# Performance work log

Measured on AMD Instinct MI355X. Metric: run time of the kernel, lower is better.

## Reference

```python
import jax, jax.numpy as jnp
import numpy as np

H = 512  # hidden size

def _lstm_layer(xseq, W_ih, W_hh, b_ih, b_hh):
    """xseq: [S,B,D]. Returns (h_seq [S,B,H], c_final [B,H]). PyTorch gate order i,f,g,o."""
    S, B, _ = xseq.shape
    # precompute input contribution for all timesteps: [S,B,4H]
    gx = jnp.einsum('sbd,gd->sbg', xseq, W_ih) + b_ih + b_hh
    h0 = jnp.zeros((B, H), xseq.dtype)
    c0 = jnp.zeros((B, H), xseq.dtype)

    def step(carry, gx_t):
        h, c = carry
        gates = gx_t + h @ W_hh.T  # [B,4H]
        i, f, g, o = jnp.split(gates, 4, axis=-1)
        c = jax.nn.sigmoid(f) * c + jax.nn.sigmoid(i) * jnp.tanh(g)
        h = jax.nn.sigmoid(o) * jnp.tanh(c)
        return (h, c), h

    (_, c_fin), h_seq = jax.lax.scan(step, (h0, c0), gx)
    return h_seq, c_fin


def setup_inputs() -> dict:
    key = jax.random.key(0)
    ks = jax.random.split(key, 12)
    V, D, L = 50257, 300, 10
    s = 0.08  # weight scale to keep gates in a sane range
    return {
        'x': jax.random.randint(ks[0], (64, 512), 0, V),
        'emb': jax.random.normal(ks[1], (V, D), jnp.float32),
        'W_ih0': s * jax.random.normal(ks[2], (4 * H, D), jnp.float32),
        'W_hh0': s * jax.random.normal(ks[3], (4 * H, H), jnp.float32),
        'b_ih0': s * jax.random.normal(ks[4], (4 * H,), jnp.float32),
        'b_hh0': s * jax.random.normal(ks[5], (4 * H,), jnp.float32),
        'W_ih1': s * jax.random.normal(ks[6], (4 * H, H), jnp.float32),
        'W_hh1': s * jax.random.normal(ks[7], (4 * H, H), jnp.float32),
        'b_ih1': s * jax.random.normal(ks[8], (4 * H,), jnp.float32),
        'b_hh1': s * jax.random.normal(ks[9], (4 * H,), jnp.float32),
        'W_out': s * jax.random.normal(ks[10], (L, H), jnp.float32),
        'b_out': s * jax.random.normal(ks[11], (L,), jnp.float32),
    }


def reference(x, emb, W_ih0, W_hh0, b_ih0, b_hh0, W_ih1, W_hh1, b_ih1, b_hh1, W_out, b_out):
    xe = emb[x]                      # [B,S,D] embedding gather
    xe = jnp.transpose(xe, (1, 0, 2))  # [S,B,D] time-major for scan
    h1, _ = _lstm_layer(xe, W_ih0, W_hh0, b_ih0, b_hh0)
    _, c2 = _lstm_layer(h1, W_ih1, W_hh1, b_ih1, b_hh1)  # c_n[-1]: [B,H]
    return c2 @ W_out.T + b_out      # [B,n_labels]
```

## Files before the change

kernel.cpp:

```cpp
#include <hip/hip_runtime.h>
#include <hip/hip_bf16.h>
#include <stdint.h>

#define BB 64
#define SS 512
#define HH 512
#define DD 300
#define DP 320

typedef __attribute__((ext_vector_type(8))) short short8;
typedef __attribute__((ext_vector_type(4))) float f32x4;

__device__ __forceinline__ unsigned short f2bf(float f) {
  unsigned u = __builtin_bit_cast(unsigned, f);
  u += 0x7fffu + ((u >> 16) & 1u);
  return (unsigned short)(u >> 16);
}
__device__ __forceinline__ float sigm(float x) { return 1.f / (1.f + __expf(-x)); }
__device__ __forceinline__ float tanh_f(float x) {
  float t = __expf(-2.f * fabsf(x));
  float r = (1.f - t) / (1.f + t);
  return x < 0.f ? -r : r;
}

__device__ __forceinline__ short8 load_frag_sc1(const unsigned short* p) {
  short8 r;
  asm volatile("global_load_dwordx4 %0, %1, off sc1" : "=v"(r) : "v"(p));
  return r;
}
__device__ __forceinline__ short8 load_frag(const unsigned short* p) {
  short8 r;
  asm volatile("global_load_dwordx4 %0, %1, off" : "=v"(r) : "v"(p));
  return r;
}

#define OFF_ARR   0u
#define OFF_EP    8192u
#define OFF_H1    16384u
#define OFF_H2    147456u
#define OFF_C2    278528u
#define OFF_XE    409600u
#define OFF_W0    21381120u
#define OFF_W1    24788992u
#define OFF_B0    28983296u
#define OFF_B1    28991488u
#define MEMSET_BYTES 278528u

__global__ void prep_weights(const float* __restrict__ Wih0, const float* __restrict__ Whh0,
                             const float* __restrict__ bih0, const float* __restrict__ bhh0,
                             const float* __restrict__ Wih1, const float* __restrict__ Whh1,
                             const float* __restrict__ bih1, const float* __restrict__ bhh1,
                             unsigned short* __restrict__ Wp0, unsigned short* __restrict__ Wp1,
                             float* __restrict__ b0p, float* __restrict__ b1p)
{
  int idx = blockIdx.x * 256 + threadIdx.x;
  int grow = idx >> 10;
  int k1 = idx & 1023;
  int l = grow & 31;
  int lb = grow >> 5;
  int gate = l >> 3;
  int orig = gate * 512 + lb * 8 + (l & 7);
  float v1 = (k1 < 512) ? Wih1[orig * 512 + k1] : Whh1[orig * 512 + (k1 - 512)];
  Wp1[idx] = f2bf(v1);
  if (k1 < 832) {
    float v0;
    if (k1 < 512)      v0 = Whh0[orig * 512 + k1];
    else if (k1 < 812) v0 = Wih0[orig * 300 + (k1 - 512)];
    else               v0 = 0.f;
    Wp0[grow * 832 + k1] = f2bf(v0);
  }
  if (k1 == 0) {
    b0p[grow] = bih0[orig] + bhh0[orig];
    b1p[grow] = bih1[orig] + bhh1[orig];
  }
}

__global__ void gather_xe(const int* __restrict__ x, const float* __restrict__ emb,
                          unsigned short* __restrict__ xe)
{
  int idx = blockIdx.x * 256 + threadIdx.x;
  int dk = idx % DP;
  int rem = idx / DP;
  int b = rem % BB;
  int t = rem / BB;
  int tok = x[b * SS + t];
  float v = (dk < DD) ? emb[(size_t)tok * DD + dk] : 0.f;
  size_t ua = (size_t)t * 20480 + (size_t)(dk >> 5) * 2048 + (size_t)(b >> 4) * 512
            + (size_t)((dk >> 3) & 3) * 128 + (size_t)(b & 15) * 8 + (dk & 7);
  xe[ua] = f2bf(v);
}

template<bool IS_L0>
__device__ __forceinline__ void scan_body(
    int blk,
    const unsigned short* __restrict__ xe,
    const unsigned short* __restrict__ Wp,
    const float* __restrict__ biasP,
    unsigned short* __restrict__ h1r,
    unsigned short* __restrict__ h2r,
    float* __restrict__ c2,
    unsigned int* cnt,
    float (&gl)[2][64][36], float (&bias_sm)[32])
{
  constexpr int K  = IS_L0 ? 832 : 1024;
  constexpr int NK = IS_L0 ? 13 : 16;

  const int tid  = threadIdx.x;
  const int lane = tid & 63;
  const int wave = tid >> 6;
  const int lrow = lane & 15;
  const int m    = wave & 3;
  const int q    = wave >> 2;
  const int lblk = IS_L0 ? blk : blk - 64;
  const int qkb  = q * NK;

  unsigned int* ep = cnt + 2048;

  if (tid < 32) bias_sm[tid] = biasP[lblk * 32 + tid];

  short8 Bf0[NK], Bf1[NK];
  {
    const unsigned short* wr0 = Wp + (size_t)(lblk * 32 + lrow) * K + qkb * 32 + (lane >> 4) * 8;
    const unsigned short* wr1 = wr0 + (size_t)16 * K;
    #pragma unroll
    for (int j = 0; j < NK; ++j) {
      Bf0[j] = *(const short8*)(wr0 + j * 32);
      Bf1[j] = *(const short8*)(wr1 + j * 32);
    }
  }
  #pragma unroll
  for (int j = 0; j < NK; ++j)
    asm volatile("" : "+v"(Bf0[j]), "+v"(Bf1[j]));

  float creg = 0.f;
  const int pb = tid >> 3;
  const int ph = tid & 7;
  const size_t hst = (size_t)(lblk >> 2) * 2048 + (size_t)(pb >> 4) * 512
                   + (size_t)(lblk & 3) * 128 + (size_t)(pb & 15) * 8 + ph;

  for (int k = 0;; ++k) {
    const bool active = IS_L0 ? (k < 512) : (k >= 1);
    short8 a[NK];

    if (IS_L0 && active) {
      const unsigned short* xet = xe + (size_t)k * 20480;
      #pragma unroll
      for (int j = 0; j < NK; ++j) {
        const int kg = qkb + j;
        if (kg >= 16)
          a[j] = load_frag(xet + (size_t)(kg - 16) * 2048 + (size_t)m * 512 + lane * 8);
      }
    }

    if (k >= 1) {
      if (blk == 0) {
        if (wave == 0) {
          const unsigned tgt = (unsigned)k * 8u;
          int guard = 0;
          for (;;) {
            unsigned v = (lane < 16)
                ? __hip_atomic_load(cnt + lane * 128, __ATOMIC_RELAXED, __HIP_MEMORY_SCOPE_AGENT)
                : tgt;
            if (__all(v >= tgt)) break;
            if (++guard > (1 << 18)) break;
            __builtin_amdgcn_s_sleep(1);
          }
          if (lane == 0)
            __hip_atomic_store(ep, (unsigned)k, __ATOMIC_RELAXED, __HIP_MEMORY_SCOPE_AGENT);
        }
      } else {
        if (wave == 0) {
          int guard = 0;
          for (;;) {
            unsigned v = __hip_atomic_load(ep, __ATOMIC_RELAXED, __HIP_MEMORY_SCOPE_AGENT);
            if (v >= (unsigned)k) break;
            if (++guard > (1 << 18)) break;
            __builtin_amdgcn_s_sleep(2);
          }
        }
      }
      __syncthreads();
    }

    if (active) {
      const int t = IS_L0 ? k : k - 1;
      const unsigned short* hA = h1r + (size_t)((IS_L0 ? (t + 1) : t) & 1) * 32768;
      const unsigned short* hB = h2r + (size_t)((t + 1) & 1) * 32768;

      #pragma unroll
      for (int j = 0; j < NK; ++j) {
        const int kg = qkb + j;
        if (kg < 16) {
          a[j] = load_frag_sc1(hA + (size_t)kg * 2048 + (size_t)m * 512 + lane * 8);
        } else if (!IS_L0) {
          a[j] = load_frag_sc1(hB + (size_t)(kg - 16) * 2048 + (size_t)m * 512 + lane * 8);
        }
      }
      asm volatile("s_waitcnt vmcnt(0)" ::: "memory");
      __builtin_amdgcn_sched_barrier(0);

      f32x4 acc0 = {0.f, 0.f, 0.f, 0.f};
      f32x4 acc1 = {0.f, 0.f, 0.f, 0.f};
      #pragma unroll
      for (int j = 0; j < NK; ++j) {
        acc0 = __builtin_amdgcn_mfma_f32_16x16x32_bf16(a[j], Bf0[j], acc0, 0, 0, 0);
        acc1 = __builtin_amdgcn_mfma_f32_16x16x32_bf16(a[j], Bf1[j], acc1, 0, 0, 0);
      }
      #pragma unroll
      for (int r = 0; r < 4; ++r) {
        const int bb = m * 16 + (lane >> 4) * 4 + r;
        gl[q][bb][lrow]      = acc0[r];
        gl[q][bb][16 + lrow] = acc1[r];
      }
      __syncthreads();

      {
        float gi = gl[0][pb][ph]      + gl[1][pb][ph]      + bias_sm[ph];
        float gf = gl[0][pb][8 + ph]  + gl[1][pb][8 + ph]  + bias_sm[8 + ph];
        float gg = gl[0][pb][16 + ph] + gl[1][pb][16 + ph] + bias_sm[16 + ph];
        float go = gl[0][pb][24 + ph] + gl[1][pb][24 + ph] + bias_sm[24 + ph];
        float iv = sigm(gi), fv = sigm(gf), ov = sigm(go), gv = tanh_f(gg);
        creg = fv * creg + iv * gv;
        float hv = ov * tanh_f(creg);
        unsigned short hb = f2bf(hv);
        unsigned pair = (unsigned)hb | ((unsigned)(unsigned short)__shfl_down((int)hb, 1) << 16);
        unsigned short* hw = (IS_L0 ? h1r : h2r) + (size_t)(t & 1) * 32768 + hst;
        if ((ph & 1) == 0)
          __hip_atomic_store((unsigned*)hw, pair, __ATOMIC_RELAXED, __HIP_MEMORY_SCOPE_AGENT);
        if (!IS_L0 && k == 512) c2[pb * HH + lblk * 8 + ph] = creg;
      }
      asm volatile("s_waitcnt vmcnt(0)" ::: "memory");
    }

    if (k == 512) break;
    __syncthreads();
    if (tid == 0)
      __hip_atomic_fetch_add(cnt + (blk >> 3) * 128, 1u, __ATOMIC_RELAXED,
                             __HIP_MEMORY_SCOPE_AGENT);
  }
}

__attribute__((amdgpu_waves_per_eu(2, 2)))
__global__ void __launch_bounds__(512)
lstm_scan(const unsigned short* __restrict__ xe,
          const unsigned short* __restrict__ Wp0,
          const unsigned short* __restrict__ Wp1,
          const float* __restrict__ b0p, const float* __restrict__ b1p,
          unsigned short* __restrict__ h1r, unsigned short* __restrict__ h2r,
          float* __restrict__ c2, unsigned int* __restrict__ cnt)
{
  __shared__ float gl[2][64][36];
  __shared__ float bias_sm[32];
  const int blk = blockIdx.x;
  if (blk < 64) scan_body<true >(blk, xe, Wp0, b0p, h1r, h2r, c2, cnt, gl, bias_sm);
  else          scan_body<false>(blk, xe, Wp1, b1p, h1r, h2r, c2, cnt, gl, bias_sm);
}

__global__ void outproj(const float* __restrict__ c2, const float* __restrict__ Wout,
                        const float* __restrict__ bout, float* __restrict__ out)
{
  int t = threadIdx.x;
  if (t >= 640) return;
  int b = t / 10, l = t % 10;
  float s = bout[l];
  #pragma unroll 8
  for (int h = 0; h < 512; ++h) s += c2[b * 512 + h] * Wout[l * 512 + h];
  out[b * 10 + l] = s;
}

extern "C" void kernel_launch(void* const* d_in, const int* in_sizes, int n_in,
                              void* d_out, int out_size, void* d_ws, size_t ws_size,
                              hipStream_t stream) {
  (void)in_sizes; (void)n_in; (void)out_size; (void)ws_size;
  const int*   x    = (const int*)  d_in[0];
  const float* emb  = (const float*)d_in[1];
  const float* Wih0 = (const float*)d_in[2];
  const float* Whh0 = (const float*)d_in[3];
  const float* bih0 = (const float*)d_in[4];
  const float* bhh0 = (const float*)d_in[5];
  const float* Wih1 = (const float*)d_in[6];
  const float* Whh1 = (const float*)d_in[7];
  const float* bih1 = (const float*)d_in[8];
  const float* bhh1 = (const float*)d_in[9];
  const float* Wout = (const float*)d_in[10];
  const float* bout = (const float*)d_in[11];
  float* out = (float*)d_out;

  char* ws = (char*)d_ws;
  unsigned int*   cnt = (unsigned int*)  (ws + OFF_ARR);
  unsigned short* h1r = (unsigned short*)(ws + OFF_H1);
  unsigned short* h2r = (unsigned short*)(ws + OFF_H2);
  float*          c2  = (float*)         (ws + OFF_C2);
  unsigned short* xe  = (unsigned short*)(ws + OFF_XE);
  unsigned short* Wp0 = (unsigned short*)(ws + OFF_W0);
  unsigned short* Wp1 = (unsigned short*)(ws + OFF_W1);
  float*          b0p = (float*)         (ws + OFF_B0);
  float*          b1p = (float*)         (ws + OFF_B1);

  hipMemsetAsync(ws, 0, MEMSET_BYTES, stream);
  prep_weights<<<8192, 256, 0, stream>>>(Wih0, Whh0, bih0, bhh0, Wih1, Whh1, bih1, bhh1,
                                         Wp0, Wp1, b0p, b1p);
  gather_xe<<<40960, 256, 0, stream>>>(x, emb, xe);
  lstm_scan<<<128, 512, 0, stream>>>(xe, Wp0, Wp1, b0p, b1p, h1r, h2r, c2, cnt);
  outproj<<<1, 640, 0, stream>>>(c2, Wout, bout, out);
}
```

Before: 2.002 ms.

## Stage per-block LSTM weights in LDS instead of holding them in registers

The packed per-block weight slice is rewritten into an MFMA-fragment-friendly layout and copied once into shared memory (64KB). Each timestep then reads the B fragments from LDS instead of keeping them pinned in VGPRs. This frees registers and drops the forced waves_per_eu setting. The cost is added LDS reads on the latency-critical recurrent step.

```diff
diff --git a/kernel.cpp b/kernel.cpp
--- a/kernel.cpp
+++ b/kernel.cpp
@@ -56,18 +56,28 @@
   int idx = blockIdx.x * 256 + threadIdx.x;
   int grow = idx >> 10;
   int k1 = idx & 1023;
-  int l = grow & 31;
-  int lb = grow >> 5;
-  int gate = l >> 3;
-  int orig = gate * 512 + lb * 8 + (l & 7);
+  int l32 = grow & 31;
+  int lblk = grow >> 5;
+  int gate = l32 >> 3;
+  int orig = gate * 512 + lblk * 8 + (l32 & 7);
+
+  const int nt   = l32 >> 4;
+  const int lrow = l32 & 15;
+  const int kb   = k1 >> 5;
+  const int lane = (((k1 >> 3) & 3) << 4) | lrow;
+  const int e    = k1 & 7;
+
   float v1 = (k1 < 512) ? Wih1[orig * 512 + k1] : Whh1[orig * 512 + (k1 - 512)];
-  Wp1[idx] = f2bf(v1);
+  size_t d1 = (size_t)lblk * 32768 + (size_t)(nt * 32 + kb) * 512 + lane * 8 + e;
+  Wp1[d1] = f2bf(v1);
+
   if (k1 < 832) {
     float v0;
     if (k1 < 512)      v0 = Whh0[orig * 512 + k1];
     else if (k1 < 812) v0 = Wih0[orig * 300 + (k1 - 512)];
     else               v0 = 0.f;
-    Wp0[grow * 832 + k1] = f2bf(v0);
+    size_t d0 = (size_t)lblk * 26624 + (size_t)(nt * 26 + kb) * 512 + lane * 8 + e;
+    Wp0[d0] = f2bf(v0);
   }
   if (k1 == 0) {
     b0p[grow] = bih0[orig] + bhh0[orig];
@@ -100,10 +110,10 @@
     unsigned short* __restrict__ h2r,
     float* __restrict__ c2,
     unsigned int* cnt,
-    float (&gl)[2][64][36], float (&bias_sm)[32])
-{
-  constexpr int K  = IS_L0 ? 832 : 1024;
-  constexpr int NK = IS_L0 ? 13 : 16;
+    unsigned short (&w_lds)[32768], float (&gl)[2][64][36], float (&bias_sm)[32])
+{
+  constexpr int NKT = IS_L0 ? 26 : 32;
+  constexpr int NK  = NKT / 2;
 
   const int tid  = threadIdx.x;
   const int lane = tid & 63;
@@ -118,19 +128,13 @@
 
   if (tid < 32) bias_sm[tid] = biasP[lblk * 32 + tid];
 
-  short8 Bf0[NK], Bf1[NK];
   {
-    const unsigned short* wr0 = Wp + (size_t)(lblk * 32 + lrow) * K + qkb * 32 + (lane >> 4) * 8;
-    const unsigned short* wr1 = wr0 + (size_t)16 * K;
-    #pragma unroll
-    for (int j = 0; j < NK; ++j) {
-      Bf0[j] = *(const short8*)(wr0 + j * 32);
-      Bf1[j] = *(const short8*)(wr1 + j * 32);
-    }
+    const short8* src = (const short8*)(Wp + (size_t)lblk * (2 * NKT * 512));
+    short8* dst = (short8*)w_lds;
+    #pragma unroll 2
+    for (int i = tid; i < NKT * 128; i += 512) dst[i] = src[i];
   }
-  #pragma unroll
-  for (int j = 0; j < NK; ++j)
-    asm volatile("" : "+v"(Bf0[j]), "+v"(Bf1[j]));
+  __syncthreads();
 
   float creg = 0.f;
   const int pb = tid >> 3;
@@ -201,10 +205,14 @@
 
       f32x4 acc0 = {0.f, 0.f, 0.f, 0.f};
       f32x4 acc1 = {0.f, 0.f, 0.f, 0.f};
+      const unsigned short* wl = w_lds + lane * 8;
       #pragma unroll
       for (int j = 0; j < NK; ++j) {
-        acc0 = __builtin_amdgcn_mfma_f32_16x16x32_bf16(a[j], Bf0[j], acc0, 0, 0, 0);
-        acc1 = __builtin_amdgcn_mfma_f32_16x16x32_bf16(a[j], Bf1[j], acc1, 0, 0, 0);
+        const int kg = qkb + j;
+        short8 b0 = *(const short8*)(wl + (size_t)kg * 512);
+        short8 b1 = *(const short8*)(wl + (size_t)(NKT + kg) * 512);
+        acc0 = __builtin_amdgcn_mfma_f32_16x16x32_bf16(a[j], b0, acc0, 0, 0, 0);
+        acc1 = __builtin_amdgcn_mfma_f32_16x16x32_bf16(a[j], b1, acc1, 0, 0, 0);
       }
       #pragma unroll
       for (int r = 0; r < 4; ++r) {
@@ -240,8 +248,7 @@
   }
 }
 
-__attribute__((amdgpu_waves_per_eu(2, 2)))
-__global__ void __launch_bounds__(512)
+__global__ void __launch_bounds__(512, 1)
 lstm_scan(const unsigned short* __restrict__ xe,
           const unsigned short* __restrict__ Wp0,
           const unsigned short* __restrict__ Wp1,
@@ -249,11 +256,12 @@
           unsigned short* __restrict__ h1r, unsigned short* __restrict__ h2r,
           float* __restrict__ c2, unsigned int* __restrict__ cnt)
 {
+  __shared__ unsigned short w_lds[32768];
   __shared__ float gl[2][64][36];
   __shared__ float bias_sm[32];
   const int blk = blockIdx.x;
-  if (blk < 64) scan_body<true >(blk, xe, Wp0, b0p, h1r, h2r, c2, cnt, gl, bias_sm);
-  else          scan_body<false>(blk, xe, Wp1, b1p, h1r, h2r, c2, cnt, gl, bias_sm);
+  if (blk < 64) scan_body<true >(blk, xe, Wp0, b0p, h1r, h2r, c2, cnt, w_lds, gl, bias_sm);
+  else          scan_body<false>(blk, xe, Wp1, b1p, h1r, h2r, c2, cnt, w_lds, gl, bias_sm);
 }
 
 __global__ void outproj(const float* __restrict__ c2, const float* __restrict__ Wout,
```

Measured after the change: 2.249 ms. 1.12x slower.
